# Kernel tuning notes

Hardware: AMD Instinct MI355X
Metric: run time of the kernel (lower is better)

Reference implementation:

```python
import jax, jax.numpy as jnp
import numpy as np
from jax import lax

FS, DW, CIN, COUT, NCLS, BATCH = 128, 8, 64, 256, 2, 512
K1, S1 = FS // 4, FS // 8          # 32, 16
L = FS * DW                        # 1024
T = (L - K1) // S1 + 1             # 63 SNN timesteps
BN_EPS = 1e-5


@jax.custom_vjp
def spike(u):
    """Heaviside spike on (v - threshold); surrogate grad exp(-|u|) (tau_grad=scale_grad=1)."""
    return (u >= 0).astype(u.dtype)

def _spike_fwd(u):
    return (u >= 0).astype(u.dtype), u

def _spike_bwd(u, g):
    return (g * jnp.exp(-jnp.abs(u)),)

spike.defvjp(_spike_fwd, _spike_bwd)


def cuba(x, threshold, current_decay, voltage_decay):
    """CUBA LIF scan. x: [N,C,T] -> binary spikes [N,C,T].
    i[t] = (1-cd)*i[t-1] + x[t]; v[t] = (1-vd)*v[t-1] + i[t]; s = v>=theta; v *= (1-s)."""
    cd, vd = 1.0 - current_decay, 1.0 - voltage_decay
    xs = jnp.moveaxis(x, -1, 0)  # [T,N,C]
    zero = jnp.zeros(x.shape[:-1], x.dtype)

    def step(carry, xt):
        i, v = carry
        i = cd * i + xt
        v = vd * v + i
        s = spike(v - threshold)
        v = v * (1.0 - s)
        return (i, v), s

    _, s = lax.scan(step, (zero, zero), xs)
    return jnp.moveaxis(s, 0, -1)


def conv1d(x, w, b, stride, pad):
    y = lax.conv_general_dilated(x, w, (stride,), [(pad, pad)],
                                 dimension_numbers=('NCH', 'OIH', 'NCH'))
    return y + b[None, :, None]


def bn(x, g, b, m, v):
    scale = g / jnp.sqrt(v + BN_EPS)
    return (x - m[None, :, None]) * scale[None, :, None] + b[None, :, None]


def setup_inputs() -> dict:
    key = jax.random.key(0)
    ks = jax.random.split(key, 12)
    return {
        'x':       jax.random.normal(ks[0], (BATCH, CIN, L), jnp.float32),
        'conv1_w': jax.random.normal(ks[1], (COUT, CIN, K1), jnp.float32) * 0.05,
        'conv1_b': jax.random.normal(ks[2], (COUT,), jnp.float32) * 0.05,
        'bn1_g':   jax.random.uniform(ks[3], (COUT,), jnp.float32, 0.5, 1.5),
        'bn1_b':   jax.random.normal(ks[4], (COUT,), jnp.float32) * 0.1,
        'bn1_m':   jax.random.normal(ks[5], (COUT,), jnp.float32) * 0.1,
        'bn1_v':   jax.random.uniform(ks[6], (COUT,), jnp.float32, 0.5, 1.5),
        'conv2_w': jax.random.normal(ks[7], (COUT, COUT, 3), jnp.float32) * 0.05,
        'conv2_b': jax.random.normal(ks[8], (COUT,), jnp.float32) * 0.05,
        'bn2_g':   jax.random.uniform(ks[9], (COUT,), jnp.float32, 0.5, 1.5),
        'bn2_b':   jax.random.normal(ks[10], (COUT,), jnp.float32) * 0.1,
        'bn2_m':   jax.random.normal(ks[11], (COUT,), jnp.float32) * 0.1,
        'bn2_v':   jax.random.uniform(jax.random.fold_in(key, 100), (COUT,), jnp.float32, 0.5, 1.5),
        'w1':      jax.random.normal(jax.random.fold_in(key, 101), (COUT, COUT), jnp.float32) * 0.1,
        'w2':      jax.random.normal(jax.random.fold_in(key, 102), (NCLS, COUT), jnp.float32) * 0.1,
    }


def reference(x, conv1_w, conv1_b, bn1_g, bn1_b, bn1_m, bn1_v,
              conv2_w, conv2_b, bn2_g, bn2_b, bn2_m, bn2_v, w1, w2):
    # CNN frontend (eval mode: BN uses running stats, dropout is identity)
    z = bn(conv1d(x, conv1_w, conv1_b, S1, 0), bn1_g, bn1_b, bn1_m, bn1_v)   # [N,COUT,T]
    z = bn(conv1d(z, conv2_w, conv2_b, 1, 1), bn2_g, bn2_b, bn2_m, bn2_v)    # [N,COUT,T]
    # CUBA Input encoder block: threshold=0.3, current_decay=0.9, voltage_decay=0.9
    z = cuba(z, 0.3, 0.9, 0.9)
    # CUBA Dense blocks (bias-free synapse per timestep + LIF): threshold=0.1, cd=1, vd=0.1
    z = cuba(jnp.einsum('oc,nct->not', w1, z), 0.1, 1.0, 0.1)
    z = cuba(jnp.einsum('oc,nct->not', w2, z), 0.1, 1.0, 0.1)
    return z  # binary spike trains [N, n_classes, T]
```

## Files before the change

kernel.cpp:

```cpp
#include <hip/hip_runtime.h>
#include <cstdint>
#include <cstddef>


typedef _Float16 half8 __attribute__((ext_vector_type(8)));
typedef float floatx4 __attribute__((ext_vector_type(4)));

__device__ __forceinline__ void split_f32(float v, _Float16& hi, _Float16& lo) {
    _Float16 h = (_Float16)v;
    hi = h;
    lo = (_Float16)((v - (float)h) * 2048.0f);
}

__global__ __launch_bounds__(256) void prep_kernel(
    const float* __restrict__ c1w, const float* __restrict__ c1b,
    const float* __restrict__ g1,  const float* __restrict__ b1,
    const float* __restrict__ m1,  const float* __restrict__ v1,
    const float* __restrict__ c2w, const float* __restrict__ c2b,
    const float* __restrict__ g2,  const float* __restrict__ b2,
    const float* __restrict__ m2,  const float* __restrict__ v2,
    const float* __restrict__ w1,
    _Float16* __restrict__ w1h, _Float16* __restrict__ w1l,
    _Float16* __restrict__ w2h, _Float16* __restrict__ w2l,
    _Float16* __restrict__ wdh, _Float16* __restrict__ wdl,
    float* __restrict__ ab1, float* __restrict__ ab2)
{
    const int id = blockIdx.x * 256 + threadIdx.x;
    if (id < 256) {
        float a1 = g1[id] / sqrtf(v1[id] + 1e-5f);
        ab1[id]       = a1;
        ab1[256 + id] = (c1b[id] - m1[id]) * a1 + b1[id];
        float a2 = g2[id] / sqrtf(v2[id] + 1e-5f);
        ab2[id]       = a2;
        ab2[256 + id] = (c2b[id] - m2[id]) * a2 + b2[id];
    }
    split_f32(w1[id], wdh[id], wdl[id]);
    for (int idx = id; idx < 256 * 2048; idx += 65536)
        split_f32(c1w[idx], w1h[idx], w1l[idx]);
    for (int idx = id; idx < 256 * 768; idx += 65536) {
        const int o  = idx / 768;
        const int r  = idx - o * 768;
        const int dt = r >> 8;
        const int c  = r & 255;
        split_f32(c2w[o * 768 + c * 3 + dt], w2h[idx], w2l[idx]);
    }
}

__global__ __launch_bounds__(256, 2) void conv1_mfma(
    const float* __restrict__ x,
    const _Float16* __restrict__ w1h, const _Float16* __restrict__ w1l,
    const float* __restrict__ ab,
    _Float16* __restrict__ z1h, _Float16* __restrict__ z1l)
{
    __shared__ _Float16 Ah[4][128][8];
    __shared__ _Float16 Al[4][128][8];
    __shared__ _Float16 Bh[4][128][8];
    __shared__ _Float16 Bl[4][128][8];

    const int tid = threadIdx.x;
    const int bm = blockIdx.x, bn = blockIdx.y;
    const int lr = tid & 127;
    const int h  = tid >> 7;

    const int am = bm * 128 + lr;
    const int an = am / 63, at = am - an * 63;
    const float*    arow  = x   + (size_t)an * 65536 + at * 16 + h * 16;
    const _Float16* bhrow = w1h + (size_t)(bn * 128 + lr) * 2048 + h * 16;
    const _Float16* blrow = w1l + (size_t)(bn * 128 + lr) * 2048 + h * 16;

    const int lane = tid & 63;
    const int wv   = tid >> 6;
    const int mw   = wv & 1, nw = wv >> 1;
    const int quad = lane >> 4;
    const int l15  = lane & 15;

    floatx4 accA[4][4] = {};
    floatx4 accB[4][4] = {};

    for (int it = 0; it < 64; ++it) {
        const float* ap = arow + it * 1024;
        float va[16];
        *(float4*)&va[0]  = *(const float4*)(ap);
        *(float4*)&va[4]  = *(const float4*)(ap + 4);
        *(float4*)&va[8]  = *(const float4*)(ap + 8);
        *(float4*)&va[12] = *(const float4*)(ap + 12);
        int4 bh0 = *(const int4*)(bhrow + it * 32);
        int4 bh1 = *(const int4*)(bhrow + it * 32 + 8);
        int4 bl0 = *(const int4*)(blrow + it * 32);
        int4 bl1 = *(const int4*)(blrow + it * 32 + 8);

        union U { _Float16 hf[8]; int4 v; };
        U c0h, c0l, c1h, c1l;
#pragma unroll
        for (int j = 0; j < 8; ++j) split_f32(va[j],     c0h.hf[j], c0l.hf[j]);
#pragma unroll
        for (int j = 0; j < 8; ++j) split_f32(va[8 + j], c1h.hf[j], c1l.hf[j]);

        __syncthreads();
        *(int4*)&Ah[2*h  ][lr][0] = c0h.v;
        *(int4*)&Ah[2*h+1][lr][0] = c1h.v;
        *(int4*)&Al[2*h  ][lr][0] = c0l.v;
        *(int4*)&Al[2*h+1][lr][0] = c1l.v;
        *(int4*)&Bh[2*h  ][lr][0] = bh0;
        *(int4*)&Bh[2*h+1][lr][0] = bh1;
        *(int4*)&Bl[2*h  ][lr][0] = bl0;
        *(int4*)&Bl[2*h+1][lr][0] = bl1;
        __syncthreads();

        half8 fah[4], fal[4], fbh[4], fbl[4];
#pragma unroll
        for (int t = 0; t < 4; ++t) {
            fah[t] = *(const half8*)&Ah[quad][mw*64 + t*16 + l15][0];
            fal[t] = *(const half8*)&Al[quad][mw*64 + t*16 + l15][0];
            fbh[t] = *(const half8*)&Bh[quad][nw*64 + t*16 + l15][0];
            fbl[t] = *(const half8*)&Bl[quad][nw*64 + t*16 + l15][0];
        }
#pragma unroll
        for (int ti = 0; ti < 4; ++ti)
#pragma unroll
            for (int tj = 0; tj < 4; ++tj) {
                accA[ti][tj] = __builtin_amdgcn_mfma_f32_16x16x32_f16(fah[ti], fbh[tj], accA[ti][tj], 0, 0, 0);
                accB[ti][tj] = __builtin_amdgcn_mfma_f32_16x16x32_f16(fah[ti], fbl[tj], accB[ti][tj], 0, 0, 0);
                accB[ti][tj] = __builtin_amdgcn_mfma_f32_16x16x32_f16(fal[ti], fbh[tj], accB[ti][tj], 0, 0, 0);
            }
    }

#pragma unroll
    for (int tj = 0; tj < 4; ++tj) {
        const int o = bn*128 + nw*64 + tj*16 + l15;
        const float alpha = ab[o], beta = ab[256 + o];
#pragma unroll
        for (int ti = 0; ti < 4; ++ti) {
            const int m0 = bm*128 + mw*64 + ti*16 + quad*4;
#pragma unroll
            for (int r = 0; r < 4; ++r) {
                float c = accA[ti][tj][r] + accB[ti][tj][r] * (1.0f/2048.0f);
                float z = c * alpha + beta;
                _Float16 zh, zl;
                split_f32(z, zh, zl);
                const size_t off = (size_t)(m0 + r) * 256 + o;
                z1h[off] = zh;
                z1l[off] = zl;
            }
        }
    }
}

__global__ __launch_bounds__(256, 2) void conv2_mfma(
    const _Float16* __restrict__ z1h, const _Float16* __restrict__ z1l,
    const _Float16* __restrict__ w2h, const _Float16* __restrict__ w2l,
    const float* __restrict__ ab, float* __restrict__ z2)
{
    __shared__ _Float16 Ah[4][128][8];
    __shared__ _Float16 Al[4][128][8];
    __shared__ _Float16 Bh[4][128][8];
    __shared__ _Float16 Bl[4][128][8];

    const int tid = threadIdx.x;
    const int bm = blockIdx.x, bn = blockIdx.y;
    const int lr = tid & 127;
    const int h  = tid >> 7;

    const int am = bm * 128 + lr;
    const int an = am / 63, at = am - an * 63;
    const _Float16* abase_h = z1h + (size_t)an * 16128;
    const _Float16* abase_l = z1l + (size_t)an * 16128;
    const _Float16* bhrow = w2h + (size_t)(bn * 128 + lr) * 768 + h * 16;
    const _Float16* blrow = w2l + (size_t)(bn * 128 + lr) * 768 + h * 16;

    const int lane = tid & 63;
    const int wv   = tid >> 6;
    const int mw   = wv & 1, nw = wv >> 1;
    const int quad = lane >> 4;
    const int l15  = lane & 15;

    floatx4 accA[4][4] = {};
    floatx4 accB[4][4] = {};

    const int4 z4 = {0, 0, 0, 0};

    for (int it = 0; it < 24; ++it) {
        const int kap0 = it * 32;
        const int dt   = kap0 >> 8;
        const int c0   = kap0 & 255;
        const int trow = at + dt - 1;
        const bool valid = (trow >= 0) && (trow < 63);
        const _Float16* aph = abase_h + trow * 256 + c0 + h * 16;
        const _Float16* apl = abase_l + trow * 256 + c0 + h * 16;
        int4 a0h = valid ? *(const int4*)(aph)     : z4;
        int4 a1h = valid ? *(const int4*)(aph + 8) : z4;
        int4 a0l = valid ? *(const int4*)(apl)     : z4;
        int4 a1l = valid ? *(const int4*)(apl + 8) : z4;
        int4 b0h = *(const int4*)(bhrow + kap0);
        int4 b1h = *(const int4*)(bhrow + kap0 + 8);
        int4 b0l = *(const int4*)(blrow + kap0);
        int4 b1l = *(const int4*)(blrow + kap0 + 8);

        __syncthreads();
        *(int4*)&Ah[2*h  ][lr][0] = a0h;
        *(int4*)&Ah[2*h+1][lr][0] = a1h;
        *(int4*)&Al[2*h  ][lr][0] = a0l;
        *(int4*)&Al[2*h+1][lr][0] = a1l;
        *(int4*)&Bh[2*h  ][lr][0] = b0h;
        *(int4*)&Bh[2*h+1][lr][0] = b1h;
        *(int4*)&Bl[2*h  ][lr][0] = b0l;
        *(int4*)&Bl[2*h+1][lr][0] = b1l;
        __syncthreads();

        half8 fah[4], fal[4], fbh[4], fbl[4];
#pragma unroll
        for (int t = 0; t < 4; ++t) {
            fah[t] = *(const half8*)&Ah[quad][mw*64 + t*16 + l15][0];
            fal[t] = *(const half8*)&Al[quad][mw*64 + t*16 + l15][0];
            fbh[t] = *(const half8*)&Bh[quad][nw*64 + t*16 + l15][0];
            fbl[t] = *(const half8*)&Bl[quad][nw*64 + t*16 + l15][0];
        }
#pragma unroll
        for (int ti = 0; ti < 4; ++ti)
#pragma unroll
            for (int tj = 0; tj < 4; ++tj) {
                accA[ti][tj] = __builtin_amdgcn_mfma_f32_16x16x32_f16(fah[ti], fbh[tj], accA[ti][tj], 0, 0, 0);
                accB[ti][tj] = __builtin_amdgcn_mfma_f32_16x16x32_f16(fah[ti], fbl[tj], accB[ti][tj], 0, 0, 0);
                accB[ti][tj] = __builtin_amdgcn_mfma_f32_16x16x32_f16(fal[ti], fbh[tj], accB[ti][tj], 0, 0, 0);
            }
    }

#pragma unroll
    for (int tj = 0; tj < 4; ++tj) {
        const int o = bn*128 + nw*64 + tj*16 + l15;
        const float alpha = ab[o], beta = ab[256 + o];
#pragma unroll
        for (int ti = 0; ti < 4; ++ti) {
            const int m0 = bm*128 + mw*64 + ti*16 + quad*4;
#pragma unroll
            for (int r = 0; r < 4; ++r) {
                float c = accA[ti][tj][r] + accB[ti][tj][r] * (1.0f/2048.0f);
                z2[(size_t)(m0 + r) * 256 + o] = c * alpha + beta;
            }
        }
    }
}

__global__ __launch_bounds__(256) void cuba1_kernel(
    const float* __restrict__ z2, _Float16* __restrict__ s1)
{
    const int n   = blockIdx.x;
    const int tid = threadIdx.x;
    const float* zrow = z2 + (size_t)n * 16128 + tid;
    _Float16*    srow = s1 + (size_t)n * 16128 + tid;
    float cur = 0.f, vol = 0.f;
    for (int t = 0; t < 63; ++t) {
        float xv = zrow[(size_t)t * 256];
        cur = 0.1f * cur + xv;
        vol = 0.1f * vol + cur;
        bool sp = (vol - 0.3f) >= 0.f;
        srow[(size_t)t * 256] = sp ? (_Float16)1.0f : (_Float16)0.0f;
        if (sp) vol = 0.f;
    }
}

__global__ __launch_bounds__(256, 2) void dense1_mfma(
    const _Float16* __restrict__ s1,
    const _Float16* __restrict__ wdh, const _Float16* __restrict__ wdl,
    float* __restrict__ y1)
{
    __shared__ _Float16 As[4][128][8];
    __shared__ _Float16 Bh[4][128][8];
    __shared__ _Float16 Bl[4][128][8];

    const int tid = threadIdx.x;
    const int bm = blockIdx.x, bn = blockIdx.y;
    const int lr = tid & 127;
    const int h  = tid >> 7;

    const _Float16* arow  = s1  + (size_t)(bm * 128 + lr) * 256 + h * 16;
    const _Float16* bhrow = wdh + (size_t)(bn * 128 + lr) * 256 + h * 16;
    const _Float16* blrow = wdl + (size_t)(bn * 128 + lr) * 256 + h * 16;

    const int lane = tid & 63;
    const int wv   = tid >> 6;
    const int mw   = wv & 1, nw = wv >> 1;
    const int quad = lane >> 4;
    const int l15  = lane & 15;

    floatx4 accA[4][4] = {};
    floatx4 accB[4][4] = {};

    for (int it = 0; it < 8; ++it) {
        const int kap0 = it * 32;
        int4 a0 = *(const int4*)(arow + kap0);
        int4 a1 = *(const int4*)(arow + kap0 + 8);
        int4 b0h = *(const int4*)(bhrow + kap0);
        int4 b1h = *(const int4*)(bhrow + kap0 + 8);
        int4 b0l = *(const int4*)(blrow + kap0);
        int4 b1l = *(const int4*)(blrow + kap0 + 8);

        __syncthreads();
        *(int4*)&As[2*h  ][lr][0] = a0;
        *(int4*)&As[2*h+1][lr][0] = a1;
        *(int4*)&Bh[2*h  ][lr][0] = b0h;
        *(int4*)&Bh[2*h+1][lr][0] = b1h;
        *(int4*)&Bl[2*h  ][lr][0] = b0l;
        *(int4*)&Bl[2*h+1][lr][0] = b1l;
        __syncthreads();

        half8 fa[4], fbh[4], fbl[4];
#pragma unroll
        for (int t = 0; t < 4; ++t) {
            fa[t]  = *(const half8*)&As[quad][mw*64 + t*16 + l15][0];
            fbh[t] = *(const half8*)&Bh[quad][nw*64 + t*16 + l15][0];
            fbl[t] = *(const half8*)&Bl[quad][nw*64 + t*16 + l15][0];
        }
#pragma unroll
        for (int ti = 0; ti < 4; ++ti)
#pragma unroll
            for (int tj = 0; tj < 4; ++tj) {
                accA[ti][tj] = __builtin_amdgcn_mfma_f32_16x16x32_f16(fa[ti], fbh[tj], accA[ti][tj], 0, 0, 0);
                accB[ti][tj] = __builtin_amdgcn_mfma_f32_16x16x32_f16(fa[ti], fbl[tj], accB[ti][tj], 0, 0, 0);
            }
    }

#pragma unroll
    for (int tj = 0; tj < 4; ++tj) {
        const int o = bn*128 + nw*64 + tj*16 + l15;
#pragma unroll
        for (int ti = 0; ti < 4; ++ti) {
            const int m0 = bm*128 + mw*64 + ti*16 + quad*4;
#pragma unroll
            for (int r = 0; r < 4; ++r)
                y1[(size_t)(m0 + r) * 256 + o] =
                    accA[ti][tj][r] + accB[ti][tj][r] * (1.0f/2048.0f);
        }
    }
}

__global__ __launch_bounds__(256) void snn_tail(
    const float* __restrict__ y1, const float* __restrict__ w2,
    float* __restrict__ out)
{
    __shared__ unsigned long long M2[256];
    __shared__ float Y[2 * 63];
    const int n   = blockIdx.x;
    const int tid = threadIdx.x;

    {
        const float* yrow = y1 + (size_t)n * 16128 + tid;
        float v = 0.f;
        unsigned long long mask2 = 0ull;
        for (int t = 0; t < 63; ++t) {
            float yv = yrow[(size_t)t * 256];
            v = 0.9f * v + yv;
            if ((v - 0.1f) >= 0.f) { mask2 |= (1ull << t); v = 0.f; }
        }
        M2[tid] = mask2;
    }
    __syncthreads();

    if (tid < 126) {
        const int cls = tid / 63;
        const int t   = tid - cls * 63;
        const float* wrow = w2 + cls * 256;
        float acc = 0.f;
#pragma unroll 4
        for (int o = 0; o < 256; ++o)
            acc += ((M2[o] >> t) & 1ull) ? wrow[o] : 0.f;
        Y[cls * 63 + t] = acc;
    }
    __syncthreads();
    if (tid < 2) {
        float v = 0.f;
        float* orow = out + (size_t)n * 126 + tid * 63;
        for (int t = 0; t < 63; ++t) {
            v = 0.9f * v + Y[tid * 63 + t];
            float u = v - 0.1f;
            float s = (u >= 0.f) ? 1.f : 0.f;
            orow[t] = s;
            v = (u >= 0.f) ? 0.f : v;
        }
    }
}

extern "C" void kernel_launch(void* const* d_in, const int* in_sizes, int n_in,
                              void* d_out, int out_size, void* d_ws, size_t ws_size,
                              hipStream_t stream)
{
    const float* x    = (const float*)d_in[0];
    const float* c1w  = (const float*)d_in[1];
    const float* c1b  = (const float*)d_in[2];
    const float* g1   = (const float*)d_in[3];
    const float* b1   = (const float*)d_in[4];
    const float* m1   = (const float*)d_in[5];
    const float* v1   = (const float*)d_in[6];
    const float* c2w  = (const float*)d_in[7];
    const float* c2b  = (const float*)d_in[8];
    const float* g2   = (const float*)d_in[9];
    const float* b2   = (const float*)d_in[10];
    const float* m2   = (const float*)d_in[11];
    const float* v2   = (const float*)d_in[12];
    const float* w1   = (const float*)d_in[13];
    const float* w2   = (const float*)d_in[14];
    float* out = (float*)d_out;

    float* ws = (float*)d_ws;
    float*    zA  = ws;
    _Float16* z1h = (_Float16*)zA;
    _Float16* z1l = (_Float16*)(zA + 4128768);
    float*    y1  = zA;
    float*    z2  = zA + 8257536;
    _Float16* s1  = (_Float16*)(z2 + 8257536);
    float*    wsp = z2 + 8257536 + 4128768;
    _Float16* w1h = (_Float16*)wsp;
    _Float16* w1l = (_Float16*)(wsp + 262144);
    _Float16* w2h = (_Float16*)(wsp + 2*262144);
    _Float16* w2l = (_Float16*)(wsp + 2*262144 + 98304);
    _Float16* wdh = (_Float16*)(wsp + 2*262144 + 2*98304);
    _Float16* wdl = (_Float16*)(wsp + 2*262144 + 2*98304 + 32768);
    float*    ab1 = wsp + 2*262144 + 2*98304 + 2*32768;
    float*    ab2 = ab1 + 512;

    prep_kernel<<<256, 256, 0, stream>>>(c1w, c1b, g1, b1, m1, v1,
                                         c2w, c2b, g2, b2, m2, v2,
                                         w1, w1h, w1l, w2h, w2l, wdh, wdl,
                                         ab1, ab2);
    conv1_mfma<<<dim3(252, 2), 256, 0, stream>>>(x, w1h, w1l, ab1, z1h, z1l);
    conv2_mfma<<<dim3(252, 2), 256, 0, stream>>>(z1h, z1l, w2h, w2l, ab2, z2);
    cuba1_kernel<<<512, 256, 0, stream>>>(z2, s1);
    dense1_mfma<<<dim3(252, 2), 256, 0, stream>>>(s1, wdh, wdl, y1);
    snn_tail<<<512, 256, 0, stream>>>(y1, w2, out);
}
```

Before: 433.3 us.

## Double K-tile per barrier in conv GEMMs and batch loads in LIF scans

The conv1 and conv2 MFMA kernels now stage a 64-wide K slice in shared memory per iteration instead of 32. This halves the number of loop iterations and __syncthreads pairs and issues more global loads per thread ahead of the barrier, at the cost of doubling LDS use (64 KB per block) and raising register pressure, which could lower occupancy. The CUBA scan kernels load 16 timesteps up front before running the serial recurrence, so memory latency overlaps instead of being paid once per step.

```diff
diff --git a/kernel.cpp b/kernel.cpp
--- a/kernel.cpp
+++ b/kernel.cpp
@@ -52,10 +52,10 @@
     const float* __restrict__ ab,
     _Float16* __restrict__ z1h, _Float16* __restrict__ z1l)
 {
-    __shared__ _Float16 Ah[4][128][8];
-    __shared__ _Float16 Al[4][128][8];
-    __shared__ _Float16 Bh[4][128][8];
-    __shared__ _Float16 Bl[4][128][8];
+    __shared__ _Float16 Ah[8][128][8];
+    __shared__ _Float16 Al[8][128][8];
+    __shared__ _Float16 Bh[8][128][8];
+    __shared__ _Float16 Bl[8][128][8];
 
     const int tid = threadIdx.x;
     const int bm = blockIdx.x, bn = blockIdx.y;
@@ -65,8 +65,8 @@
     const int am = bm * 128 + lr;
     const int an = am / 63, at = am - an * 63;
     const float*    arow  = x   + (size_t)an * 65536 + at * 16 + h * 16;
-    const _Float16* bhrow = w1h + (size_t)(bn * 128 + lr) * 2048 + h * 16;
-    const _Float16* blrow = w1l + (size_t)(bn * 128 + lr) * 2048 + h * 16;
+    const _Float16* bhrow = w1h + (size_t)(bn * 128 + lr) * 2048 + h * 32;
+    const _Float16* blrow = w1l + (size_t)(bn * 128 + lr) * 2048 + h * 32;
 
     const int lane = tid & 63;
     const int wv   = tid >> 6;
@@ -77,52 +77,71 @@
     floatx4 accA[4][4] = {};
     floatx4 accB[4][4] = {};
 
-    for (int it = 0; it < 64; ++it) {
-        const float* ap = arow + it * 1024;
-        float va[16];
-        *(float4*)&va[0]  = *(const float4*)(ap);
-        *(float4*)&va[4]  = *(const float4*)(ap + 4);
-        *(float4*)&va[8]  = *(const float4*)(ap + 8);
-        *(float4*)&va[12] = *(const float4*)(ap + 12);
-        int4 bh0 = *(const int4*)(bhrow + it * 32);
-        int4 bh1 = *(const int4*)(bhrow + it * 32 + 8);
-        int4 bl0 = *(const int4*)(blrow + it * 32);
-        int4 bl1 = *(const int4*)(blrow + it * 32 + 8);
+    for (int it = 0; it < 32; ++it) {
+        const float* ap0 = arow + (size_t)(2 * it)     * 1024;
+        const float* ap1 = arow + (size_t)(2 * it + 1) * 1024;
+        float va[16], vb[16];
+        *(float4*)&va[0]  = *(const float4*)(ap0);
+        *(float4*)&va[4]  = *(const float4*)(ap0 + 4);
+        *(float4*)&va[8]  = *(const float4*)(ap0 + 8);
+        *(float4*)&va[12] = *(const float4*)(ap0 + 12);
+        *(float4*)&vb[0]  = *(const float4*)(ap1);
+        *(float4*)&vb[4]  = *(const float4*)(ap1 + 4);
+        *(float4*)&vb[8]  = *(const float4*)(ap1 + 8);
+        *(float4*)&vb[12] = *(const float4*)(ap1 + 12);
+        int4 bhv[4], blv[4];
+#pragma unroll
+        for (int q = 0; q < 4; ++q) {
+            bhv[q] = *(const int4*)(bhrow + it * 64 + q * 8);
+            blv[q] = *(const int4*)(blrow + it * 64 + q * 8);
+        }
 
         union U { _Float16 hf[8]; int4 v; };
-        U c0h, c0l, c1h, c1l;
-#pragma unroll
-        for (int j = 0; j < 8; ++j) split_f32(va[j],     c0h.hf[j], c0l.hf[j]);
-#pragma unroll
-        for (int j = 0; j < 8; ++j) split_f32(va[8 + j], c1h.hf[j], c1l.hf[j]);
-
-        __syncthreads();
-        *(int4*)&Ah[2*h  ][lr][0] = c0h.v;
-        *(int4*)&Ah[2*h+1][lr][0] = c1h.v;
-        *(int4*)&Al[2*h  ][lr][0] = c0l.v;
-        *(int4*)&Al[2*h+1][lr][0] = c1l.v;
-        *(int4*)&Bh[2*h  ][lr][0] = bh0;
-        *(int4*)&Bh[2*h+1][lr][0] = bh1;
-        *(int4*)&Bl[2*h  ][lr][0] = bl0;
-        *(int4*)&Bl[2*h+1][lr][0] = bl1;
-        __syncthreads();
-
-        half8 fah[4], fal[4], fbh[4], fbl[4];
-#pragma unroll
-        for (int t = 0; t < 4; ++t) {
-            fah[t] = *(const half8*)&Ah[quad][mw*64 + t*16 + l15][0];
-            fal[t] = *(const half8*)&Al[quad][mw*64 + t*16 + l15][0];
-            fbh[t] = *(const half8*)&Bh[quad][nw*64 + t*16 + l15][0];
-            fbl[t] = *(const half8*)&Bl[quad][nw*64 + t*16 + l15][0];
-        }
-#pragma unroll
-        for (int ti = 0; ti < 4; ++ti)
-#pragma unroll
-            for (int tj = 0; tj < 4; ++tj) {
-                accA[ti][tj] = __builtin_amdgcn_mfma_f32_16x16x32_f16(fah[ti], fbh[tj], accA[ti][tj], 0, 0, 0);
-                accB[ti][tj] = __builtin_amdgcn_mfma_f32_16x16x32_f16(fah[ti], fbl[tj], accB[ti][tj], 0, 0, 0);
-                accB[ti][tj] = __builtin_amdgcn_mfma_f32_16x16x32_f16(fal[ti], fbh[tj], accB[ti][tj], 0, 0, 0);
-            }
+        U a0h, a0l, a1h, a1l, a2h, a2l, a3h, a3l;
+#pragma unroll
+        for (int j = 0; j < 8; ++j) split_f32(va[j],     a0h.hf[j], a0l.hf[j]);
+#pragma unroll
+        for (int j = 0; j < 8; ++j) split_f32(va[8 + j], a1h.hf[j], a1l.hf[j]);
+#pragma unroll
+        for (int j = 0; j < 8; ++j) split_f32(vb[j],     a2h.hf[j], a2l.hf[j]);
+#pragma unroll
+        for (int j = 0; j < 8; ++j) split_f32(vb[8 + j], a3h.hf[j], a3l.hf[j]);
+
+        __syncthreads();
+        *(int4*)&Ah[h*2    ][lr][0] = a0h.v;
+        *(int4*)&Ah[h*2 + 1][lr][0] = a1h.v;
+        *(int4*)&Ah[h*2 + 4][lr][0] = a2h.v;
+        *(int4*)&Ah[h*2 + 5][lr][0] = a3h.v;
+        *(int4*)&Al[h*2    ][lr][0] = a0l.v;
+        *(int4*)&Al[h*2 + 1][lr][0] = a1l.v;
+        *(int4*)&Al[h*2 + 4][lr][0] = a2l.v;
+        *(int4*)&Al[h*2 + 5][lr][0] = a3l.v;
+#pragma unroll
+        for (int q = 0; q < 4; ++q) {
+            *(int4*)&Bh[h*4 + q][lr][0] = bhv[q];
+            *(int4*)&Bl[h*4 + q][lr][0] = blv[q];
+        }
+        __syncthreads();
+
+#pragma unroll
+        for (int g = 0; g < 2; ++g) {
+            half8 fah[4], fal[4], fbh[4], fbl[4];
+#pragma unroll
+            for (int t = 0; t < 4; ++t) {
+                fah[t] = *(const half8*)&Ah[g*4 + quad][mw*64 + t*16 + l15][0];
+                fal[t] = *(const half8*)&Al[g*4 + quad][mw*64 + t*16 + l15][0];
+                fbh[t] = *(const half8*)&Bh[g*4 + quad][nw*64 + t*16 + l15][0];
+                fbl[t] = *(const half8*)&Bl[g*4 + quad][nw*64 + t*16 + l15][0];
+            }
+#pragma unroll
+            for (int ti = 0; ti < 4; ++ti)
+#pragma unroll
+                for (int tj = 0; tj < 4; ++tj) {
+                    accA[ti][tj] = __builtin_amdgcn_mfma_f32_16x16x32_f16(fah[ti], fbh[tj], accA[ti][tj], 0, 0, 0);
+                    accB[ti][tj] = __builtin_amdgcn_mfma_f32_16x16x32_f16(fah[ti], fbl[tj], accB[ti][tj], 0, 0, 0);
+                    accB[ti][tj] = __builtin_amdgcn_mfma_f32_16x16x32_f16(fal[ti], fbh[tj], accB[ti][tj], 0, 0, 0);
+                }
+        }
     }
 
 #pragma unroll
@@ -151,10 +170,10 @@
     const _Float16* __restrict__ w2h, const _Float16* __restrict__ w2l,
     const float* __restrict__ ab, float* __restrict__ z2)
 {
-    __shared__ _Float16 Ah[4][128][8];
-    __shared__ _Float16 Al[4][128][8];
-    __shared__ _Float16 Bh[4][128][8];
-    __shared__ _Float16 Bl[4][128][8];
+    __shared__ _Float16 Ah[8][128][8];
+    __shared__ _Float16 Al[8][128][8];
+    __shared__ _Float16 Bh[8][128][8];
+    __shared__ _Float16 Bl[8][128][8];
 
     const int tid = threadIdx.x;
     const int bm = blockIdx.x, bn = blockIdx.y;
@@ -165,8 +184,8 @@
     const int an = am / 63, at = am - an * 63;
     const _Float16* abase_h = z1h + (size_t)an * 16128;
     const _Float16* abase_l = z1l + (size_t)an * 16128;
-    const _Float16* bhrow = w2h + (size_t)(bn * 128 + lr) * 768 + h * 16;
-    const _Float16* blrow = w2l + (size_t)(bn * 128 + lr) * 768 + h * 16;
+    const _Float16* bhrow = w2h + (size_t)(bn * 128 + lr) * 768 + h * 32;
+    const _Float16* blrow = w2l + (size_t)(bn * 128 + lr) * 768 + h * 32;
 
     const int lane = tid & 63;
     const int wv   = tid >> 6;
@@ -179,50 +198,52 @@
 
     const int4 z4 = {0, 0, 0, 0};
 
-    for (int it = 0; it < 24; ++it) {
-        const int kap0 = it * 32;
-        const int dt   = kap0 >> 8;
-        const int c0   = kap0 & 255;
+    for (int it = 0; it < 12; ++it) {
+        const int k0 = it * 64;
+        const int dt = k0 >> 8;
+        const int c0 = (k0 & 255) + h * 32;
         const int trow = at + dt - 1;
         const bool valid = (trow >= 0) && (trow < 63);
-        const _Float16* aph = abase_h + trow * 256 + c0 + h * 16;
-        const _Float16* apl = abase_l + trow * 256 + c0 + h * 16;
-        int4 a0h = valid ? *(const int4*)(aph)     : z4;
-        int4 a1h = valid ? *(const int4*)(aph + 8) : z4;
-        int4 a0l = valid ? *(const int4*)(apl)     : z4;
-        int4 a1l = valid ? *(const int4*)(apl + 8) : z4;
-        int4 b0h = *(const int4*)(bhrow + kap0);
-        int4 b1h = *(const int4*)(bhrow + kap0 + 8);
-        int4 b0l = *(const int4*)(blrow + kap0);
-        int4 b1l = *(const int4*)(blrow + kap0 + 8);
-
-        __syncthreads();
-        *(int4*)&Ah[2*h  ][lr][0] = a0h;
-        *(int4*)&Ah[2*h+1][lr][0] = a1h;
-        *(int4*)&Al[2*h  ][lr][0] = a0l;
-        *(int4*)&Al[2*h+1][lr][0] = a1l;
-        *(int4*)&Bh[2*h  ][lr][0] = b0h;
-        *(int4*)&Bh[2*h+1][lr][0] = b1h;
-        *(int4*)&Bl[2*h  ][lr][0] = b0l;
-        *(int4*)&Bl[2*h+1][lr][0] = b1l;
-        __syncthreads();
-
-        half8 fah[4], fal[4], fbh[4], fbl[4];
-#pragma unroll
-        for (int t = 0; t < 4; ++t) {
-            fah[t] = *(const half8*)&Ah[quad][mw*64 + t*16 + l15][0];
-            fal[t] = *(const half8*)&Al[quad][mw*64 + t*16 + l15][0];
-            fbh[t] = *(const half8*)&Bh[quad][nw*64 + t*16 + l15][0];
-            fbl[t] = *(const half8*)&Bl[quad][nw*64 + t*16 + l15][0];
-        }
-#pragma unroll
-        for (int ti = 0; ti < 4; ++ti)
-#pragma unroll
-            for (int tj = 0; tj < 4; ++tj) {
-                accA[ti][tj] = __builtin_amdgcn_mfma_f32_16x16x32_f16(fah[ti], fbh[tj], accA[ti][tj], 0, 0, 0);
-                accB[ti][tj] = __builtin_amdgcn_mfma_f32_16x16x32_f16(fah[ti], fbl[tj], accB[ti][tj], 0, 0, 0);
-                accB[ti][tj] = __builtin_amdgcn_mfma_f32_16x16x32_f16(fal[ti], fbh[tj], accB[ti][tj], 0, 0, 0);
-            }
+        const _Float16* aph = abase_h + trow * 256 + c0;
+        const _Float16* apl = abase_l + trow * 256 + c0;
+        int4 ahv[4], alv[4], bhv[4], blv[4];
+#pragma unroll
+        for (int q = 0; q < 4; ++q) {
+            ahv[q] = valid ? *(const int4*)(aph + q * 8) : z4;
+            alv[q] = valid ? *(const int4*)(apl + q * 8) : z4;
+            bhv[q] = *(const int4*)(bhrow + it * 64 + q * 8);
+            blv[q] = *(const int4*)(blrow + it * 64 + q * 8);
+        }
+
+        __syncthreads();
+#pragma unroll
+        for (int q = 0; q < 4; ++q) {
+            *(int4*)&Ah[h*4 + q][lr][0] = ahv[q];
+            *(int4*)&Al[h*4 + q][lr][0] = alv[q];
+            *(int4*)&Bh[h*4 + q][lr][0] = bhv[q];
+            *(int4*)&Bl[h*4 + q][lr][0] = blv[q];
+        }
+        __syncthreads();
+
+#pragma unroll
+        for (int g = 0; g < 2; ++g) {
+            half8 fah[4], fal[4], fbh[4], fbl[4];
+#pragma unroll
+            for (int t = 0; t < 4; ++t) {
+                fah[t] = *(const half8*)&Ah[g*4 + quad][mw*64 + t*16 + l15][0];
+                fal[t] = *(const half8*)&Al[g*4 + quad][mw*64 + t*16 + l15][0];
+                fbh[t] = *(const half8*)&Bh[g*4 + quad][nw*64 + t*16 + l15][0];
+                fbl[t] = *(const half8*)&Bl[g*4 + quad][nw*64 + t*16 + l15][0];
+            }
+#pragma unroll
+            for (int ti = 0; ti < 4; ++ti)
+#pragma unroll
+                for (int tj = 0; tj < 4; ++tj) {
+                    accA[ti][tj] = __builtin_amdgcn_mfma_f32_16x16x32_f16(fah[ti], fbh[tj], accA[ti][tj], 0, 0, 0);
+                    accB[ti][tj] = __builtin_amdgcn_mfma_f32_16x16x32_f16(fah[ti], fbl[tj], accB[ti][tj], 0, 0, 0);
+                    accB[ti][tj] = __builtin_amdgcn_mfma_f32_16x16x32_f16(fal[ti], fbh[tj], accB[ti][tj], 0, 0, 0);
+                }
+        }
     }
 
 #pragma unroll
@@ -249,13 +270,23 @@
     const float* zrow = z2 + (size_t)n * 16128 + tid;
     _Float16*    srow = s1 + (size_t)n * 16128 + tid;
     float cur = 0.f, vol = 0.f;
-    for (int t = 0; t < 63; ++t) {
-        float xv = zrow[(size_t)t * 256];
-        cur = 0.1f * cur + xv;
-        vol = 0.1f * vol + cur;
-        bool sp = (vol - 0.3f) >= 0.f;
-        srow[(size_t)t * 256] = sp ? (_Float16)1.0f : (_Float16)0.0f;
-        if (sp) vol = 0.f;
+    for (int tb = 0; tb < 4; ++tb) {
+        const int base = tb * 16;
+        const int nT   = (tb == 3) ? 15 : 16;
+        float xv[16];
+#pragma unroll
+        for (int j = 0; j < 16; ++j)
+            if (j < nT) xv[j] = zrow[(size_t)(base + j) * 256];
+#pragma unroll
+        for (int j = 0; j < 16; ++j) {
+            if (j < nT) {
+                cur = 0.1f * cur + xv[j];
+                vol = 0.1f * vol + cur;
+                bool sp = (vol - 0.3f) >= 0.f;
+                srow[(size_t)(base + j) * 256] = sp ? (_Float16)1.0f : (_Float16)0.0f;
+                if (sp) vol = 0.f;
+            }
+        }
     }
 }
 
@@ -347,10 +378,20 @@
         const float* yrow = y1 + (size_t)n * 16128 + tid;
         float v = 0.f;
         unsigned long long mask2 = 0ull;
-        for (int t = 0; t < 63; ++t) {
-            float yv = yrow[(size_t)t * 256];
-            v = 0.9f * v + yv;
-            if ((v - 0.1f) >= 0.f) { mask2 |= (1ull << t); v = 0.f; }
+        for (int tb = 0; tb < 4; ++tb) {
+            const int base = tb * 16;
+            const int nT   = (tb == 3) ? 15 : 16;
+            float yv[16];
+#pragma unroll
+            for (int j = 0; j < 16; ++j)
+                if (j < nT) yv[j] = yrow[(size_t)(base + j) * 256];
+#pragma unroll
+            for (int j = 0; j < 16; ++j) {
+                if (j < nT) {
+                    v = 0.9f * v + yv[j];
+                    if ((v - 0.1f) >= 0.f) { mask2 |= (1ull << (base + j)); v = 0.f; }
+                }
+            }
         }
         M2[tid] = mask2;
     }
```

Measured after the change: 598.3 us. 38.1% more time.
